# Performance work log

Hardware: AMD Instinct MI355X
Metric: run time of the kernel (lower is better)

The kernel has to match this reference:

```python
import jax, jax.numpy as jnp
import numpy as np

B, NB, T, C, H = 4, 256, 33, 512, 8
HD = C // H
SCALE = HD ** -0.5


def setup_inputs() -> dict:
    key = jax.random.key(0)
    ks = jax.random.split(key, 8)
    x = jax.random.normal(ks[0], (B, NB * T, C), jnp.float32)
    m = jax.random.randint(ks[1], (NB, T, T), 0, 2)
    eye = jnp.eye(T, dtype=m.dtype)
    attn_mask = jnp.maximum(m, eye[None, :, :]).astype(jnp.int32)  # diag always attendable
    edge_feats = jax.random.normal(ks[2], (NB, T, T, 4), jnp.float32)
    Wqkv = jax.random.normal(ks[3], (3 * C, C), jnp.float32) * (C ** -0.5)
    bqkv = jnp.zeros((3 * C,), jnp.float32)
    Wproj = jax.random.normal(ks[4], (C, C), jnp.float32) * (C ** -0.5)
    bproj = jnp.zeros((C,), jnp.float32)
    Wgate = jax.random.normal(ks[5], (H, 4), jnp.float32) * 0.01  # init.normal_(std=0.01)
    bgate = jnp.zeros((H,), jnp.float32)
    return dict(x=x, attn_mask=attn_mask, edge_feats=edge_feats,
                Wqkv=Wqkv, bqkv=bqkv, Wproj=Wproj, bproj=bproj,
                Wgate=Wgate, bgate=bgate)


def reference(x, attn_mask, edge_feats, Wqkv, bqkv, Wproj, bproj, Wgate, bgate):
    Bq, N, Cd = x.shape
    x_blk = x.reshape(Bq, NB, T, Cd)                         # (B,nb,T,C)
    qkv = x_blk @ Wqkv.T + bqkv                              # (B,nb,T,3C)
    q, k, v = jnp.split(qkv, 3, axis=-1)
    q = q.reshape(Bq, NB, T, H, HD)
    k = k.reshape(Bq, NB, T, H, HD)
    v = v.reshape(Bq, NB, T, H, HD)
    scores = jnp.einsum('bnqhd,bnkhd->bnqkh', q, k) * SCALE  # (B,nb,T,T,H)

    # physics bias: copy edge_feats[...,:4], overwrite diagonal to (0,0,0,1)
    bias = jnp.broadcast_to(edge_feats[None, ..., :4], (Bq, NB, T, T, 4))
    eye = jnp.eye(T, dtype=bool)[None, None, :, :, None]
    diag_vals = jnp.array([0.0, 0.0, 0.0, 1.0], dtype=bias.dtype)
    bias = jnp.where(eye, diag_vals, bias)

    scores = scores + bias[..., 3:4]                         # broadcast over heads
    mask_e = (attn_mask[None, :, :, :, None] != 0)           # (1,nb,T,T,1)
    scores = jnp.where(mask_e, scores, -jnp.inf)
    probs = jax.nn.softmax(scores, axis=3)                   # softmax over keys

    gates = bias @ Wgate.T + bgate                           # (B,nb,T,T,H)
    gates = jnp.where(mask_e, gates, 0.0)
    cw = probs + gates                                       # combined weights

    out = jnp.einsum('bnqkh,bnkhd->bnqhd', cw, v).reshape(Bq, NB, T, Cd)
    out = out @ Wproj.T + bproj
    return out.reshape(Bq, NB * T, Cd)
```

## Files before the change

### kernel.cpp

```cpp
#include <hip/hip_runtime.h>

typedef _Float16 half8 __attribute__((ext_vector_type(8)));
typedef _Float16 half4v __attribute__((ext_vector_type(4)));
typedef float floatx4 __attribute__((ext_vector_type(4)));
typedef unsigned uint4v __attribute__((ext_vector_type(4)));
typedef unsigned uint2v __attribute__((ext_vector_type(2)));

#define KDIM 512

__device__ __forceinline__ void gll16(const _Float16* g, void* l) {
  __builtin_amdgcn_global_load_lds((const __attribute__((address_space(1))) void*)g,
                                   (__attribute__((address_space(3))) void*)l, 16, 0, 0);
}

__device__ __forceinline__ unsigned pack2(float a, float b) {
  return __builtin_bit_cast(unsigned, __builtin_amdgcn_cvt_pkrtz(a, b));
}

__global__ void cvt_all(const float* __restrict__ x, const float* __restrict__ wq,
                        const float* __restrict__ wp, _Float16* __restrict__ xh,
                        _Float16* __restrict__ wqh, _Float16* __restrict__ wph) {
  long stride = (long)gridDim.x * blockDim.x;
  long t0 = (long)blockIdx.x * blockDim.x + threadIdx.x;
  for (long i = t0; i < 17301504L/4; i += stride) {
    float4 v = ((const float4*)x)[i];
    half4v h; h[0]=(_Float16)v.x; h[1]=(_Float16)v.y; h[2]=(_Float16)v.z; h[3]=(_Float16)v.w;
    ((half4v*)xh)[i] = h;
  }
  for (long i = t0; i < 786432L/4; i += stride) {
    float4 v = ((const float4*)wq)[i];
    half4v h; h[0]=(_Float16)v.x; h[1]=(_Float16)v.y; h[2]=(_Float16)v.z; h[3]=(_Float16)v.w;
    ((half4v*)wqh)[i] = h;
  }
  for (long i = t0; i < 262144L/4; i += stride) {
    float4 v = ((const float4*)wp)[i];
    half4v h; h[0]=(_Float16)v.x; h[1]=(_Float16)v.y; h[2]=(_Float16)v.z; h[3]=(_Float16)v.w;
    ((half4v*)wph)[i] = h;
  }
}

template<int NN, bool OUTF16>
__global__ __launch_bounds__(256, 2) void gemm_bt(const _Float16* __restrict__ A,
    const _Float16* __restrict__ Bw, const float* __restrict__ bias,
    void* __restrict__ Cout) {
  __shared__ __attribute__((aligned(16))) _Float16 As[128*64];
  __shared__ __attribute__((aligned(16))) _Float16 Bs[128*64];
  const int ntile = NN / 128;
  int bid = blockIdx.x;
  int mt = bid / ntile, nt = bid % ntile;
  int tid = threadIdx.x;
  int lane = tid & 63;
  int w = tid >> 6, wr = w >> 1, wc = w & 1;
  int g = lane >> 4, c = lane & 15;
  long arow0 = (long)mt * 128;
  int bcol0 = nt * 128;
  floatx4 acc[4][4];
#pragma unroll
  for (int i = 0; i < 4; i++)
#pragma unroll
    for (int j = 0; j < 4; j++) acc[i][j] = (floatx4)0.0f;

  int wbase = tid & ~63;
  for (int kt = 0; kt < KDIM / 64; ++kt) {
    if (kt) __syncthreads();
    int k0 = kt * 64;
#pragma unroll
    for (int j = 0; j < 4; ++j) {
      int idx = j * 256 + tid;
      int row = idx >> 3;
      int sc = (idx & 7) ^ (row & 7);
      gll16(A + ((arow0 + row) * KDIM + k0 + sc * 8), (char*)As + (j * 256 + wbase) * 16);
      gll16(Bw + ((long)(bcol0 + row) * KDIM + k0 + sc * 8), (char*)Bs + (j * 256 + wbase) * 16);
    }
    __syncthreads();
#pragma unroll
    for (int ks = 0; ks < 2; ++ks) {
      half8 af[4], bf[4];
      int cb = ks * 64 + g * 16;
#pragma unroll
      for (int i = 0; i < 4; ++i) {
        int ra = wr * 64 + i * 16 + c;
        af[i] = *(const half8*)((const char*)As + ra * 128 + (cb ^ ((ra & 7) << 4)));
        int rb = wc * 64 + i * 16 + c;
        bf[i] = *(const half8*)((const char*)Bs + rb * 128 + (cb ^ ((rb & 7) << 4)));
      }
#pragma unroll
      for (int mi = 0; mi < 4; mi++)
#pragma unroll
        for (int ni = 0; ni < 4; ni++)
          acc[mi][ni] = __builtin_amdgcn_mfma_f32_16x16x32_f16(af[mi], bf[ni], acc[mi][ni], 0, 0, 0);
    }
  }
  long crow0 = arow0 + wr * 64;
  int ccol0 = bcol0 + wc * 64;
#pragma unroll
  for (int mi = 0; mi < 4; mi++) {
#pragma unroll
    for (int ni = 0; ni < 4; ni++) {
      int col = ccol0 + ni * 16 + c;
      float bv = bias[col];
#pragma unroll
      for (int j = 0; j < 4; j++) {
        long r = crow0 + mi * 16 + g * 4 + j;
        float v = acc[mi][ni][j] + bv;
        if (OUTF16) ((_Float16*)Cout)[r * NN + col] = (_Float16)v;
        else        ((float*)Cout)[r * NN + col] = v;
      }
    }
  }
}

__global__ __launch_bounds__(256, 4) void attn_mid(const _Float16* __restrict__ qkv,
    const int* __restrict__ amask, const float* __restrict__ ef,
    const float* __restrict__ Wg, const float* __restrict__ bg,
    _Float16* __restrict__ aout) {
  __shared__ __attribute__((aligned(16))) half4v efT[48][42];
  __shared__ __attribute__((aligned(16))) _Float16 outb[4][33][88];
  __shared__ unsigned long long mrow[48];
  int blk = blockIdx.x;
  int nb = blk & 255;
  long R0 = (long)blk * 33;
  int tid = threadIdx.x;
  int lane = tid & 63, w = tid >> 6;
  int g = lane >> 4, c = lane & 15;

  if (tid < 48) {
    unsigned long long bits = 0;
    if (tid < 33) {
      const int* mp = amask + ((long)nb * 33 + tid) * 33;
      for (int k = 0; k < 33; k++) if (mp[k]) bits |= (1ull << k);
    }
    mrow[tid] = bits;
  }
  for (int u = tid; u < 48 * 42; u += 256) {
    int k = u / 42, q = u - k * 42;
    half4v hv; hv[0] = (_Float16)0.f; hv[1] = (_Float16)0.f; hv[2] = (_Float16)0.f; hv[3] = (_Float16)0.f;
    if (q < 33 && k < 33) {
      if (q == k) hv[3] = (_Float16)1.0f;
      else {
        float4 e4 = *(const float4*)(ef + (((long)nb * 33 + q) * 33 + k) * 4);
        hv[0] = (_Float16)e4.x; hv[1] = (_Float16)e4.y; hv[2] = (_Float16)e4.z; hv[3] = (_Float16)e4.w;
      }
    }
    efT[k][q] = hv;
  }
  __syncthreads();

  for (int hh = 0; hh < 2; ++hh) {
    int h = w + 4 * hh;
    float wg0 = Wg[h * 4 + 0], wg1 = Wg[h * 4 + 1], wg2 = Wg[h * 4 + 2], wg3 = Wg[h * 4 + 3];
    float bgh = bg[h];
    half8 qf[3][2], kf[3][2];
#pragma unroll
    for (int t3 = 0; t3 < 3; ++t3) {
      int t = t3 * 16 + c;
      long tr = R0 + (t < 33 ? t : 0);
#pragma unroll
      for (int ks = 0; ks < 2; ++ks) {
        int d0 = ks * 32 + g * 8;
        qf[t3][ks] = *(const half8*)(qkv + tr * 1536 + h * 64 + d0);
        kf[t3][ks] = *(const half8*)(qkv + tr * 1536 + 512 + h * 64 + d0);
      }
    }
    floatx4 s[3][3];
#pragma unroll
    for (int kt = 0; kt < 3; kt++)
#pragma unroll
      for (int qt = 0; qt < 3; qt++) s[kt][qt] = (floatx4)0.0f;
#pragma unroll
    for (int ks = 0; ks < 2; ++ks)
#pragma unroll
      for (int kt = 0; kt < 3; kt++)
#pragma unroll
        for (int qt = 0; qt < 3; qt++)
          s[kt][qt] = __builtin_amdgcn_mfma_f32_16x16x32_f16(kf[kt][ks], qf[qt][ks], s[kt][qt], 0, 0, 0);

    unsigned pk[2][3][2];
    float cw32[3];
#pragma unroll
    for (int qt = 0; qt < 3; qt++) {
      int q = qt * 16 + c;
      unsigned long long mb = mrow[q];
      float sv[3][4];
#pragma unroll
      for (int kt = 0; kt < 3; kt++)
#pragma unroll
        for (int j = 0; j < 4; j++) {
          int k = kt * 16 + 4 * g + j;
          float e3 = (float)efT[k][q][3];
          bool mk = (mb >> k) & 1;
          sv[kt][j] = mk ? s[kt][qt][j] * 0.125f + e3 : -1e30f;
        }
      float m = sv[0][0];
#pragma unroll
      for (int kt = 0; kt < 3; kt++)
#pragma unroll
        for (int j = 0; j < 4; j++) m = fmaxf(m, sv[kt][j]);
      m = fmaxf(m, __shfl_xor(m, 16, 64));
      m = fmaxf(m, __shfl_xor(m, 32, 64));
      float p[3][4], sum = 0.f;
#pragma unroll
      for (int kt = 0; kt < 3; kt++)
#pragma unroll
        for (int j = 0; j < 4; j++) { p[kt][j] = __expf(sv[kt][j] - m); sum += p[kt][j]; }
      sum += __shfl_xor(sum, 16, 64);
      sum += __shfl_xor(sum, 32, 64);
      float inv = __builtin_amdgcn_rcpf(sum);
      float cw[3][4];
#pragma unroll
      for (int kt = 0; kt < 3; kt++)
#pragma unroll
        for (int j = 0; j < 4; j++) {
          int k = kt * 16 + 4 * g + j;
          bool mk = (mb >> k) & 1;
          half4v e = efT[k][q];
          float gate = (float)e[0] * wg0 + (float)e[1] * wg1 + (float)e[2] * wg2 + (float)e[3] * wg3 + bgh;
          cw[kt][j] = mk ? p[kt][j] * inv + gate : 0.0f;
        }
#pragma unroll
      for (int kt = 0; kt < 2; kt++)
#pragma unroll
        for (int jp = 0; jp < 2; jp++) pk[kt][qt][jp] = pack2(cw[kt][2 * jp], cw[kt][2 * jp + 1]);
      cw32[qt] = cw[2][0];
    }

    half8 pb[3];
#pragma unroll
    for (int qt = 0; qt < 3; qt++) {
      uint4v d;
#pragma unroll
      for (int w2 = 0; w2 < 4; w2++) {
        int srcl = (((g & 1) * 2 + (w2 >> 1)) << 4) | c;
        unsigned v0 = (unsigned)__shfl((int)pk[0][qt][w2 & 1], srcl, 64);
        unsigned v1 = (unsigned)__shfl((int)pk[1][qt][w2 & 1], srcl, 64);
        d[w2] = (g >> 1) ? v1 : v0;
      }
      pb[qt] = __builtin_bit_cast(half8, d);
    }

    floatx4 o[4][3];
#pragma unroll
    for (int dt = 0; dt < 4; dt++)
#pragma unroll
      for (int qt = 0; qt < 3; qt++) o[dt][qt] = (floatx4)0.0f;
#pragma unroll
    for (int dh = 0; dh < 2; dh++) {
      half8 vf[2];
#pragma unroll
      for (int di = 0; di < 2; di++) {
        int dt = dh * 2 + di;
        half8 v;
#pragma unroll
        for (int e = 0; e < 8; e++)
          v[e] = qkv[(R0 + g * 8 + e) * 1536 + 1024 + h * 64 + dt * 16 + c];
        vf[di] = v;
      }
#pragma unroll
      for (int di = 0; di < 2; di++)
#pragma unroll
        for (int qt = 0; qt < 3; qt++)
          o[dh * 2 + di][qt] = __builtin_amdgcn_mfma_f32_16x16x32_f16(vf[di], pb[qt], o[dh * 2 + di][qt], 0, 0, 0);
    }
    float p32[3];
#pragma unroll
    for (int qt = 0; qt < 3; qt++) p32[qt] = __shfl(cw32[qt], c, 64);
#pragma unroll
    for (int dt = 0; dt < 4; dt++) {
      half4v v32 = *(const half4v*)(qkv + (R0 + 32) * 1536 + 1024 + h * 64 + dt * 16 + 4 * g);
#pragma unroll
      for (int qt = 0; qt < 3; qt++)
#pragma unroll
        for (int j = 0; j < 4; j++) o[dt][qt][j] += (float)v32[j] * p32[qt];
    }

#pragma unroll
    for (int qt = 0; qt < 3; qt++) {
      int q = qt * 16 + c;
      if (q < 33) {
#pragma unroll
        for (int dt = 0; dt < 4; dt++) {
          uint2v uu;
          uu[0] = pack2(o[dt][qt][0], o[dt][qt][1]);
          uu[1] = pack2(o[dt][qt][2], o[dt][qt][3]);
          *(uint2v*)&outb[w][q][dt * 16 + 4 * g] = uu;
        }
      }
    }
#pragma unroll
    for (int r0 = 0; r0 < 5; ++r0) {
      int q = r0 * 8 + (lane >> 3);
      if (q < 33) {
        half8 vv = *(const half8*)&outb[w][q][(lane & 7) * 8];
        *(half8*)(aout + (R0 + q) * 512 + h * 64 + (lane & 7) * 8) = vv;
      }
    }
  }
}

extern "C" void kernel_launch(void* const* d_in, const int* in_sizes, int n_in,
                              void* d_out, int out_size, void* d_ws, size_t ws_size,
                              hipStream_t stream) {
  const float* x  = (const float*)d_in[0];
  const int*   am = (const int*)d_in[1];
  const float* ef = (const float*)d_in[2];
  const float* Wq = (const float*)d_in[3];
  const float* bq = (const float*)d_in[4];
  const float* Wp = (const float*)d_in[5];
  const float* bp = (const float*)d_in[6];
  const float* Wg = (const float*)d_in[7];
  const float* bg = (const float*)d_in[8];
  char* ws = (char*)d_ws;
  _Float16* xh   = (_Float16*)(ws);
  _Float16* wqh  = (_Float16*)(ws + 34603008L);
  _Float16* wph  = (_Float16*)(ws + 36175872L);
  _Float16* qkv  = (_Float16*)(ws + 36700160L);
  _Float16* aout = (_Float16*)(ws + 140509184L);

  hipLaunchKernelGGL(cvt_all, dim3(2048), dim3(256), 0, stream, x, Wq, Wp, xh, wqh, wph);
  hipLaunchKernelGGL((gemm_bt<1536, true>), dim3(264 * 12), dim3(256), 0, stream, xh, wqh, bq, (void*)qkv);
  hipLaunchKernelGGL(attn_mid, dim3(1024), dim3(256), 0, stream, qkv, am, ef, Wg, bg, aout);
  hipLaunchKernelGGL((gemm_bt<512, false>), dim3(264 * 4), dim3(256), 0, stream, aout, wph, bp, (float*)d_out);
}
```

Before: 155.1 us.

## Fuse x fp32-to-fp16 conversion into QKV GEMM and remap blocks across XCDs

Removes the separate pass that converted the whole activation tensor x to fp16. The QKV GEMM now loads fp32 rows into registers, converts them, and writes them to swizzled LDS, prefetching the next k-tile during the MFMA loop. Both GEMMs also remap block indices so that neighbouring M tiles land on different XCDs while sharing N tiles for L2 reuse. The trade-off is doubled A-load bytes inside the GEMM and register-staged rather than direct-to-LDS A loads, in exchange for skipping a full write and re-read of the fp16 copy of x.

```diff
diff --git a/kernel.cpp b/kernel.cpp
--- a/kernel.cpp
+++ b/kernel.cpp
@@ -17,16 +17,10 @@
   return __builtin_bit_cast(unsigned, __builtin_amdgcn_cvt_pkrtz(a, b));
 }
 
-__global__ void cvt_all(const float* __restrict__ x, const float* __restrict__ wq,
-                        const float* __restrict__ wp, _Float16* __restrict__ xh,
-                        _Float16* __restrict__ wqh, _Float16* __restrict__ wph) {
+__global__ void cvt_w(const float* __restrict__ wq, const float* __restrict__ wp,
+                      _Float16* __restrict__ wqh, _Float16* __restrict__ wph) {
   long stride = (long)gridDim.x * blockDim.x;
   long t0 = (long)blockIdx.x * blockDim.x + threadIdx.x;
-  for (long i = t0; i < 17301504L/4; i += stride) {
-    float4 v = ((const float4*)x)[i];
-    half4v h; h[0]=(_Float16)v.x; h[1]=(_Float16)v.y; h[2]=(_Float16)v.z; h[3]=(_Float16)v.w;
-    ((half4v*)xh)[i] = h;
-  }
   for (long i = t0; i < 786432L/4; i += stride) {
     float4 v = ((const float4*)wq)[i];
     half4v h; h[0]=(_Float16)v.x; h[1]=(_Float16)v.y; h[2]=(_Float16)v.z; h[3]=(_Float16)v.w;
@@ -37,6 +31,106 @@
     half4v h; h[0]=(_Float16)v.x; h[1]=(_Float16)v.y; h[2]=(_Float16)v.z; h[3]=(_Float16)v.w;
     ((half4v*)wph)[i] = h;
   }
+}
+
+__global__ __launch_bounds__(256, 2) void gemm1_f32a(const float* __restrict__ X,
+    const _Float16* __restrict__ Bw, const float* __restrict__ bias,
+    _Float16* __restrict__ Cout) {
+  __shared__ __attribute__((aligned(16))) _Float16 As[128 * 64];
+  __shared__ __attribute__((aligned(16))) _Float16 Bs[128 * 64];
+  const int NN = 1536, ntile = 12;
+  int bid = blockIdx.x;
+  int xcd = bid & 7, idx = bid >> 3;
+  int mt = (idx / ntile) * 8 + xcd;
+  int nt = idx % ntile;
+  long arow0 = (long)mt * 128;
+  int bcol0 = nt * 128;
+  int tid = threadIdx.x;
+  int lane = tid & 63, w = tid >> 6;
+  int wr = w >> 1, wc = w & 1;
+  int g = lane >> 4, c = lane & 15;
+  int wbase = tid & ~63;
+
+  float4 ra[4][2];
+  auto LOADA = [&](int kt) {
+#pragma unroll
+    for (int j = 0; j < 4; ++j) {
+      int id4 = j * 256 + tid;
+      int row = id4 >> 3, s = id4 & 7;
+      const float* p = X + (arow0 + row) * 512L + kt * 64 + s * 8;
+      ra[j][0] = *(const float4*)p;
+      ra[j][1] = *(const float4*)(p + 4);
+    }
+  };
+  auto WRITEA = [&]() {
+#pragma unroll
+    for (int j = 0; j < 4; ++j) {
+      int id4 = j * 256 + tid;
+      int row = id4 >> 3, s = id4 & 7;
+      half8 h;
+      h[0]=(_Float16)ra[j][0].x; h[1]=(_Float16)ra[j][0].y;
+      h[2]=(_Float16)ra[j][0].z; h[3]=(_Float16)ra[j][0].w;
+      h[4]=(_Float16)ra[j][1].x; h[5]=(_Float16)ra[j][1].y;
+      h[6]=(_Float16)ra[j][1].z; h[7]=(_Float16)ra[j][1].w;
+      *(half8*)((char*)As + row * 128 + ((s ^ (row & 7)) << 4)) = h;
+    }
+  };
+  auto STAGEB = [&](int kt) {
+#pragma unroll
+    for (int j = 0; j < 4; ++j) {
+      int id4 = j * 256 + tid;
+      int row = id4 >> 3;
+      int sc = (id4 & 7) ^ (row & 7);
+      gll16(Bw + ((long)(bcol0 + row) * 512 + kt * 64 + sc * 8),
+            (char*)Bs + (j * 256 + wbase) * 16);
+    }
+  };
+
+  floatx4 acc[4][4];
+#pragma unroll
+  for (int i = 0; i < 4; i++)
+#pragma unroll
+    for (int j = 0; j < 4; j++) acc[i][j] = (floatx4)0.0f;
+
+  LOADA(0);
+  for (int kt = 0; kt < 8; ++kt) {
+    if (kt) __syncthreads();
+    WRITEA();
+    STAGEB(kt);
+    __syncthreads();
+    if (kt < 7) LOADA(kt + 1);
+#pragma unroll
+    for (int ks = 0; ks < 2; ++ks) {
+      half8 af[4], bf[4];
+      int cb = ks * 64 + g * 16;
+#pragma unroll
+      for (int i = 0; i < 4; ++i) {
+        int ra_ = wr * 64 + i * 16 + c;
+        af[i] = *(const half8*)((const char*)As + ra_ * 128 + (cb ^ ((ra_ & 7) << 4)));
+        int rb = wc * 64 + i * 16 + c;
+        bf[i] = *(const half8*)((const char*)Bs + rb * 128 + (cb ^ ((rb & 7) << 4)));
+      }
+#pragma unroll
+      for (int mi = 0; mi < 4; mi++)
+#pragma unroll
+        for (int ni = 0; ni < 4; ni++)
+          acc[mi][ni] = __builtin_amdgcn_mfma_f32_16x16x32_f16(af[mi], bf[ni], acc[mi][ni], 0, 0, 0);
+    }
+  }
+  long crow0 = arow0 + wr * 64;
+  int ccol0 = bcol0 + wc * 64;
+#pragma unroll
+  for (int mi = 0; mi < 4; mi++)
+#pragma unroll
+    for (int ni = 0; ni < 4; ni++) {
+      int col = ccol0 + ni * 16 + c;
+      float bv = bias[col];
+#pragma unroll
+      for (int j = 0; j < 4; j++) {
+        long r = crow0 + mi * 16 + g * 4 + j;
+        Cout[r * NN + col] = (_Float16)(acc[mi][ni][j] + bv);
+      }
+    }
 }
 
 template<int NN, bool OUTF16>
@@ -47,7 +141,9 @@
   __shared__ __attribute__((aligned(16))) _Float16 Bs[128*64];
   const int ntile = NN / 128;
   int bid = blockIdx.x;
-  int mt = bid / ntile, nt = bid % ntile;
+  int xcd = bid & 7, idx = bid >> 3;
+  int mt = (idx / ntile) * 8 + xcd;
+  int nt = idx % ntile;
   int tid = threadIdx.x;
   int lane = tid & 63;
   int w = tid >> 6, wr = w >> 1, wc = w & 1;
@@ -66,9 +162,9 @@
     int k0 = kt * 64;
 #pragma unroll
     for (int j = 0; j < 4; ++j) {
-      int idx = j * 256 + tid;
-      int row = idx >> 3;
-      int sc = (idx & 7) ^ (row & 7);
+      int idx4 = j * 256 + tid;
+      int row = idx4 >> 3;
+      int sc = (idx4 & 7) ^ (row & 7);
       gll16(A + ((arow0 + row) * KDIM + k0 + sc * 8), (char*)As + (j * 256 + wbase) * 16);
       gll16(Bw + ((long)(bcol0 + row) * KDIM + k0 + sc * 8), (char*)Bs + (j * 256 + wbase) * 16);
     }
@@ -310,14 +406,13 @@
   const float* Wg = (const float*)d_in[7];
   const float* bg = (const float*)d_in[8];
   char* ws = (char*)d_ws;
-  _Float16* xh   = (_Float16*)(ws);
-  _Float16* wqh  = (_Float16*)(ws + 34603008L);
-  _Float16* wph  = (_Float16*)(ws + 36175872L);
-  _Float16* qkv  = (_Float16*)(ws + 36700160L);
-  _Float16* aout = (_Float16*)(ws + 140509184L);
-
-  hipLaunchKernelGGL(cvt_all, dim3(2048), dim3(256), 0, stream, x, Wq, Wp, xh, wqh, wph);
-  hipLaunchKernelGGL((gemm_bt<1536, true>), dim3(264 * 12), dim3(256), 0, stream, xh, wqh, bq, (void*)qkv);
+  _Float16* wqh  = (_Float16*)(ws);
+  _Float16* wph  = (_Float16*)(ws + 2097152L);
+  _Float16* qkv  = (_Float16*)(ws + 4194304L);
+  _Float16* aout = (_Float16*)(ws + 108003328L);
+
+  hipLaunchKernelGGL(cvt_w, dim3(512), dim3(256), 0, stream, Wq, Wp, wqh, wph);
+  hipLaunchKernelGGL(gemm1_f32a, dim3(3168), dim3(256), 0, stream, x, wqh, bq, qkv);
   hipLaunchKernelGGL(attn_mid, dim3(1024), dim3(256), 0, stream, qkv, am, ef, Wg, bg, aout);
-  hipLaunchKernelGGL((gemm_bt<512, false>), dim3(264 * 4), dim3(256), 0, stream, aout, wph, bp, (float*)d_out);
-}
+  hipLaunchKernelGGL((gemm_bt<512, false>), dim3(1056), dim3(256), 0, stream, aout, wph, bp, (float*)d_out);
+}
```

Result: no change. 152.9 us (-1.4%).
